# Kernel tuning notes

Measured on AMD Instinct MI355X. Metric: run time of the kernel, lower is better.

Reference implementation:

```python
import jax, jax.numpy as jnp
import numpy as np

N = 50000
E = 800000
HID = 128
OUT = 64
HEADS = 4
NEG_SLOPE = 0.2


def gat_layer(x, edge_index, W, att_src, att_dst, bias):
    """PyG-style GATConv: shared linear for src/dst, additive attention,
    self-loops, segment softmax over incoming edges, concat heads + bias."""
    n = x.shape[0]
    H, C = att_src.shape
    # add self loops (PyG default add_self_loops=True)
    loops = jnp.arange(n, dtype=edge_index.dtype)
    src = jnp.concatenate([edge_index[0], loops])  # message sources j
    dst = jnp.concatenate([edge_index[1], loops])  # aggregation targets i
    xl = (x @ W).reshape(n, H, C)                  # [N,H,C]
    a_s = jnp.einsum('nhc,hc->nh', xl, att_src)    # [N,H]
    a_d = jnp.einsum('nhc,hc->nh', xl, att_dst)    # [N,H]
    e = jax.nn.leaky_relu(a_s[src] + a_d[dst], NEG_SLOPE)   # [E',H]
    m = jax.ops.segment_max(e, dst, num_segments=n)         # stable softmax
    e = jnp.exp(e - m[dst])
    denom = jax.ops.segment_sum(e, dst, num_segments=n)
    alpha = e / (denom[dst] + 1e-16)                        # [E',H]
    msg = xl[src] * alpha[:, :, None]                       # [E',H,C]
    out = jax.ops.segment_sum(msg, dst, num_segments=n)     # [N,H,C]
    return out.reshape(n, H * C) + bias


def setup_inputs() -> dict:
    key = jax.random.key(0)
    ks = jax.random.split(key, 16)
    C = HID // HEADS  # per-head channels = 32
    x = jax.random.normal(ks[0], (N, HID), dtype=jnp.float32)
    edge_indices = jax.random.randint(ks[1], (3, 2, E), 0, N, dtype=jnp.int32)
    s = 0.1
    inp = {
        'x': x,
        'edge_indices': edge_indices,
        'W1': jax.random.normal(ks[2], (HID, HEADS * C), dtype=jnp.float32) * s,
        'as1': jax.random.normal(ks[3], (HEADS, C), dtype=jnp.float32) * s,
        'ad1': jax.random.normal(ks[4], (HEADS, C), dtype=jnp.float32) * s,
        'b1': jnp.zeros((HEADS * C,), dtype=jnp.float32),
        'W2': jax.random.normal(ks[5], (HID, HEADS * C), dtype=jnp.float32) * s,
        'as2': jax.random.normal(ks[6], (HEADS, C), dtype=jnp.float32) * s,
        'ad2': jax.random.normal(ks[7], (HEADS, C), dtype=jnp.float32) * s,
        'b2': jnp.zeros((HEADS * C,), dtype=jnp.float32),
        'W3': jax.random.normal(ks[8], (HID, OUT), dtype=jnp.float32) * s,
        'as3': jax.random.normal(ks[9], (1, OUT), dtype=jnp.float32) * s,
        'ad3': jax.random.normal(ks[10], (1, OUT), dtype=jnp.float32) * s,
        'b3': jnp.zeros((OUT,), dtype=jnp.float32),
    }
    return inp


def reference(x, edge_indices, W1, as1, ad1, b1, W2, as2, ad2, b2, W3, as3, ad3, b3):
    h = jax.nn.relu(gat_layer(x, edge_indices[0], W1, as1, ad1, b1))
    h = jax.nn.relu(gat_layer(h, edge_indices[1], W2, as2, ad2, b2))
    out = gat_layer(h, edge_indices[2], W3, as3, ad3, b3)  # no ReLU on last layer
    return out
```

## Files before the change

kernel.cpp:

```cpp
#include <hip/hip_runtime.h>

typedef unsigned short u16;
typedef unsigned int u32;

#define HID 128

static inline int cdiv(long long a, int b) { return (int)((a + b - 1) / b); }

__device__ __forceinline__ float bfbits(u32 u) { union { u32 u; float f; } c; c.u = u; return c.f; }
__device__ __forceinline__ u16 f2bf(float f) {
  union { float f; u32 u; } c; c.f = f;
  u32 u = c.u;
  return (u16)((u + 0x7fffu + ((u >> 16) & 1u)) >> 16);
}
__device__ __forceinline__ u32 pack2bf(float a, float b) {
  return (u32)f2bf(a) | ((u32)f2bf(b) << 16);
}

template <int COUT, int HEADS>
__global__ __launch_bounds__(256) void gemm_attn(
    const float* __restrict__ Hin, const float* __restrict__ W,
    const float* __restrict__ attS, const float* __restrict__ attD,
    u16* __restrict__ XL, float* __restrict__ aS, float* __restrict__ aD, int n) {
  constexpr int TN = COUT / 8;
  constexpr int TM = 256 / TN;
  constexpr int MT = TM * 8;
  constexpr int HALF = COUT / 2;
  constexpr int C = COUT / HEADS;
  constexpr bool SAMEHEAD = (HALF < C);

  __shared__ float xs[32][MT + 4];
  __shared__ float ws[32][COUT];

  int t = threadIdx.x;
  int tx = t % TN, ty = t / TN;
  int rowBase = blockIdx.x * MT;

  float acc[8][8];
#pragma unroll
  for (int r = 0; r < 8; ++r)
#pragma unroll
    for (int c = 0; c < 8; ++c) acc[r][c] = 0.f;

  for (int kb = 0; kb < 4; ++kb) {
    __syncthreads();
    {
      int kg = (t & 7) * 4;
#pragma unroll
      for (int pass = 0; pass < MT / 32; ++pass) {
        int rr = pass * 32 + (t >> 3);
        int grow = rowBase + rr;
        float4 v = make_float4(0.f, 0.f, 0.f, 0.f);
        if (grow < n) v = *(const float4*)(Hin + (size_t)grow * HID + kb * 32 + kg);
        xs[kg + 0][rr] = v.x;
        xs[kg + 1][rr] = v.y;
        xs[kg + 2][rr] = v.z;
        xs[kg + 3][rr] = v.w;
      }
    }
    {
      constexpr int WF = 32 * COUT / 256;
      const float* wp = W + (size_t)kb * 32 * COUT;
      float* wsf = &ws[0][0];
#pragma unroll
      for (int u = 0; u < WF; u += 4) {
        int idx = t * WF + u;
        *(float4*)(wsf + idx) = *(const float4*)(wp + idx);
      }
    }
    __syncthreads();
#pragma unroll 8
    for (int k = 0; k < 32; ++k) {
      const float4 xv0 = *(const float4*)&xs[k][ty * 8];
      const float4 xv1 = *(const float4*)&xs[k][ty * 8 + 4];
      const float4 wv0 = *(const float4*)&ws[k][tx * 4];
      const float4 wv1 = *(const float4*)&ws[k][HALF + tx * 4];
      const float xr[8] = {xv0.x, xv0.y, xv0.z, xv0.w, xv1.x, xv1.y, xv1.z, xv1.w};
      const float wc[8] = {wv0.x, wv0.y, wv0.z, wv0.w, wv1.x, wv1.y, wv1.z, wv1.w};
#pragma unroll
      for (int r = 0; r < 8; ++r)
#pragma unroll
        for (int c = 0; c < 8; ++c) acc[r][c] += xr[r] * wc[c];
    }
  }

  float sv[8], dv[8];
#pragma unroll
  for (int j = 0; j < 4; ++j) {
    sv[j] = attS[tx * 4 + j];
    sv[4 + j] = attS[HALF + tx * 4 + j];
    dv[j] = attD[tx * 4 + j];
    dv[4 + j] = attD[HALF + tx * 4 + j];
  }
  int row0 = rowBase + ty * 8;
  int hlo = (tx * 4) / C;
  int hhi = (HALF + tx * 4) / C;
  u32* XLo = (u32*)XL;
#pragma unroll
  for (int r = 0; r < 8; ++r) {
    int row = row0 + r;
    bool ok = (row < n);
    if (ok) {
      u32 lo01 = pack2bf(acc[r][0], acc[r][1]);
      u32 lo23 = pack2bf(acc[r][2], acc[r][3]);
      u32 hi01 = pack2bf(acc[r][4], acc[r][5]);
      u32 hi23 = pack2bf(acc[r][6], acc[r][7]);
      *(uint2*)(XLo + (size_t)row * (COUT / 2) + tx * 2) = make_uint2(lo01, lo23);
      *(uint2*)(XLo + (size_t)row * (COUT / 2) + COUT / 4 + tx * 2) = make_uint2(hi01, hi23);
    }
    float pslo = acc[r][0] * sv[0] + acc[r][1] * sv[1] + acc[r][2] * sv[2] + acc[r][3] * sv[3];
    float pshi = acc[r][4] * sv[4] + acc[r][5] * sv[5] + acc[r][6] * sv[6] + acc[r][7] * sv[7];
    float pdlo = acc[r][0] * dv[0] + acc[r][1] * dv[1] + acc[r][2] * dv[2] + acc[r][3] * dv[3];
    float pdhi = acc[r][4] * dv[4] + acc[r][5] * dv[5] + acc[r][6] * dv[6] + acc[r][7] * dv[7];
    if (SAMEHEAD) { pslo += pshi; pdlo += pdhi; }
#pragma unroll
    for (int mk = 1; mk < 8; mk <<= 1) {
      pslo += __shfl_xor(pslo, mk);
      pdlo += __shfl_xor(pdlo, mk);
      if (!SAMEHEAD) {
        pshi += __shfl_xor(pshi, mk);
        pdhi += __shfl_xor(pdhi, mk);
      }
    }
    if (((tx & 7) == 0) && ok) {
      aS[(size_t)row * HEADS + hlo] = pslo;
      aD[(size_t)row * HEADS + hlo] = pdlo;
      if (!SAMEHEAD) {
        aS[(size_t)row * HEADS + hhi] = pshi;
        aD[(size_t)row * HEADS + hhi] = pdhi;
      }
    }
  }
}

#define PSTR 16

__global__ __launch_bounds__(256) void bucket_hist(const int* __restrict__ ei,
                                                   int* __restrict__ cntP,
                                                   int e4, int rem, int E, int NB) {
  int L = blockIdx.y;
  const int* dst = ei + (size_t)(2 * L + 1) * E;
  __shared__ int cnt[256];
  int t = threadIdx.x;
  cnt[t] = 0;
  __syncthreads();
  int gbase = blockIdx.x * 1024 + t;
#pragma unroll
  for (int u = 0; u < 4; ++u) {
    int g = gbase + u * 256;
    if (g < e4) {
      int4 d = *(const int4*)(dst + g * 4);
      atomicAdd(&cnt[d.x >> 8], 1);
      atomicAdd(&cnt[d.y >> 8], 1);
      atomicAdd(&cnt[d.z >> 8], 1);
      atomicAdd(&cnt[d.w >> 8], 1);
    }
  }
  if (blockIdx.x == 0 && t < rem) atomicAdd(&cnt[dst[e4 * 4 + t] >> 8], 1);
  __syncthreads();
  int c = cnt[t];
  if (t < NB && c > 0) atomicAdd(&cntP[(L * NB + t) * PSTR], c);
}

__global__ __launch_bounds__(256) void bucket_scan(const int* __restrict__ cntP,
                                                   int* __restrict__ bucketOff,
                                                   int* __restrict__ curP, int NB, int E) {
  int L = blockIdx.x;
  int t = threadIdx.x;
  int lane = t & 63, wid = t >> 6;
  __shared__ int wpart[4];
  int v = (t < NB) ? cntP[(L * NB + t) * PSTR] : 0;
  int inc = v;
#pragma unroll
  for (int off = 1; off < 64; off <<= 1) {
    int w = __shfl_up(inc, (unsigned)off, 64);
    if (lane >= off) inc += w;
  }
  if (lane == 63) wpart[wid] = inc;
  __syncthreads();
  if (t == 0) {
    int a = 0;
#pragma unroll
    for (int k = 0; k < 4; ++k) { int tmp = wpart[k]; wpart[k] = a; a += tmp; }
  }
  __syncthreads();
  int ex = wpart[wid] + inc - v;
  if (t < NB) {
    bucketOff[L * (NB + 1) + t] = ex;
    curP[(L * NB + t) * PSTR] = ex;
  }
  if (t == 0) bucketOff[L * (NB + 1) + NB] = E;
}

__global__ __launch_bounds__(256) void bucket_scatter(const int* __restrict__ ei,
                                                      int* __restrict__ curP,
                                                      int2* __restrict__ pairsAll,
                                                      int e4, int rem, int E, int NB) {
  int L = blockIdx.y;
  const int* src = ei + (size_t)(2 * L) * E;
  const int* dst = src + E;
  int2* pairs = pairsAll + (size_t)L * E;
  __shared__ int cnt[256];
  __shared__ int baseS[256];
  int t = threadIdx.x;
  cnt[t] = 0;
  __syncthreads();

  int gbase = blockIdx.x * 1024 + t;
  int4 dv[4], sv[4];
  bool val[4];
#pragma unroll
  for (int u = 0; u < 4; ++u) {
    int g = gbase + u * 256;
    val[u] = (g < e4);
    if (val[u]) {
      dv[u] = *(const int4*)(dst + g * 4);
      sv[u] = *(const int4*)(src + g * 4);
      atomicAdd(&cnt[dv[u].x >> 8], 1);
      atomicAdd(&cnt[dv[u].y >> 8], 1);
      atomicAdd(&cnt[dv[u].z >> 8], 1);
      atomicAdd(&cnt[dv[u].w >> 8], 1);
    }
  }
  int tailS = 0, tailD = 0;
  bool hasTail = (blockIdx.x == 0 && t < rem);
  if (hasTail) {
    tailD = dst[e4 * 4 + t];
    tailS = src[e4 * 4 + t];
    atomicAdd(&cnt[tailD >> 8], 1);
  }
  __syncthreads();
  int c = cnt[t];
  if (t < NB && c > 0) baseS[t] = atomicAdd(&curP[(L * NB + t) * PSTR], c);
  __syncthreads();
  cnt[t] = 0;
  __syncthreads();
#pragma unroll
  for (int u = 0; u < 4; ++u) {
    if (val[u]) {
      int b, p;
      b = dv[u].x >> 8; p = atomicAdd(&cnt[b], 1); pairs[baseS[b] + p] = make_int2(sv[u].x, dv[u].x);
      b = dv[u].y >> 8; p = atomicAdd(&cnt[b], 1); pairs[baseS[b] + p] = make_int2(sv[u].y, dv[u].y);
      b = dv[u].z >> 8; p = atomicAdd(&cnt[b], 1); pairs[baseS[b] + p] = make_int2(sv[u].z, dv[u].z);
      b = dv[u].w >> 8; p = atomicAdd(&cnt[b], 1); pairs[baseS[b] + p] = make_int2(sv[u].w, dv[u].w);
    }
  }
  if (hasTail) {
    int b = tailD >> 8;
    int p = atomicAdd(&cnt[b], 1);
    pairs[baseS[b] + p] = make_int2(tailS, tailD);
  }
}

__global__ __launch_bounds__(256) void csr_finalize(const int2* __restrict__ pairsAll,
                                                    const int* __restrict__ bucketOff,
                                                    int* __restrict__ indptrAll,
                                                    int* __restrict__ srcIdxAll,
                                                    int N, int E, int NB) {
  int L = blockIdx.y, b = blockIdx.x;
  const int2* pairs = pairsAll + (size_t)L * E;
  int* indptr = indptrAll + (size_t)L * (N + 1);
  int* srcL = srcIdxAll + (size_t)L * (E + N);
  int base = b << 8;
  int nodes = min(256, N - base);
  int p0 = bucketOff[L * (NB + 1) + b];
  int p1 = bucketOff[L * (NB + 1) + b + 1];

  __shared__ int cnt[256];
  __shared__ int wpart[4];
  int t = threadIdx.x;
  int lane = t & 63, wid = t >> 6;
  cnt[t] = 0;
  __syncthreads();

  for (int i = p0 + t; i < p1; i += 256) atomicAdd(&cnt[pairs[i].y - base], 1);
  __syncthreads();

  int v = (t < nodes) ? cnt[t] + 1 : 0;
  int inc = v;
#pragma unroll
  for (int off = 1; off < 64; off <<= 1) {
    int w = __shfl_up(inc, (unsigned)off, 64);
    if (lane >= off) inc += w;
  }
  if (lane == 63) wpart[wid] = inc;
  __syncthreads();
  if (t == 0) {
    int a = 0;
#pragma unroll
    for (int k = 0; k < 4; ++k) { int tmp = wpart[k]; wpart[k] = a; a += tmp; }
  }
  __syncthreads();
  int ex = wpart[wid] + inc - v;
  __syncthreads();
  if (t < nodes) {
    int segStart = p0 + base + ex;
    indptr[base + t] = segStart;
    srcL[segStart] = base + t;
    cnt[t] = segStart + 1;
  }
  if (b == NB - 1 && t == 0) indptr[N] = E + N;
  __syncthreads();

  for (int i = p0 + t; i < p1; i += 256) {
    int2 pr = pairs[i];
    int p = atomicAdd(&cnt[pr.y - base], 1);
    srcL[p] = pr.x;
  }
}

template <int COUT, int HEADS, bool RELU>
__global__ __launch_bounds__(256) void aggregate(
    const u16* __restrict__ XL, const float* __restrict__ aS, const float* __restrict__ aD,
    const int* __restrict__ indptr, const int* __restrict__ srcIdx,
    const float* __restrict__ bias, float* __restrict__ outF, int n) {
  constexpr int VPL = COUT / 64;
  constexpr int C = COUT / HEADS;
  int wave = (blockIdx.x * blockDim.x + threadIdx.x) >> 6;
  if (wave >= n) return;
  int lane = threadIdx.x & 63;
  int i = wave;
  int col = lane * VPL;
  int h = col / C;
  float ad = aD[i * HEADS + h];
  float s = 0.f, acc0 = 0.f, acc1 = 0.f;
  int e0 = indptr[i], e1 = indptr[i + 1];
  int idx = e0;
  const u32* XL32 = (const u32*)XL;

  for (; idx + 8 <= e1; idx += 8) {
    int j[8];
#pragma unroll
    for (int u = 0; u < 8; ++u) j[u] = srcIdx[idx + u];
    float a[8];
#pragma unroll
    for (int u = 0; u < 8; ++u) a[u] = aS[j[u] * HEADS + h];
    if (VPL == 2) {
      u32 px[8];
#pragma unroll
      for (int u = 0; u < 8; ++u) px[u] = XL32[j[u] * (COUT / 2) + lane];
#pragma unroll
      for (int u = 0; u < 8; ++u) {
        float l = a[u] + ad;
        l = (l >= 0.f) ? l : 0.2f * l;
        float el = __expf(fminf(l, 60.f));
        s += el;
        acc0 += el * bfbits(px[u] << 16);
        acc1 += el * bfbits(px[u] & 0xffff0000u);
      }
    } else {
      u16 px[8];
#pragma unroll
      for (int u = 0; u < 8; ++u) px[u] = XL[j[u] * COUT + lane];
#pragma unroll
      for (int u = 0; u < 8; ++u) {
        float l = a[u] + ad;
        l = (l >= 0.f) ? l : 0.2f * l;
        float el = __expf(fminf(l, 60.f));
        s += el;
        acc0 += el * bfbits(((u32)px[u]) << 16);
      }
    }
  }
  for (; idx < e1; ++idx) {
    int j = srcIdx[idx];
    float l = aS[j * HEADS + h] + ad;
    l = (l >= 0.f) ? l : 0.2f * l;
    float el = __expf(fminf(l, 60.f));
    s += el;
    if (VPL == 2) {
      u32 px = XL32[j * (COUT / 2) + lane];
      acc0 += el * bfbits(px << 16);
      acc1 += el * bfbits(px & 0xffff0000u);
    } else {
      acc0 += el * bfbits(((u32)XL[j * COUT + lane]) << 16);
    }
  }

  float inv = 1.f / (s + 1e-16f);
  float o0 = acc0 * inv + bias[col];
  if (RELU) o0 = fmaxf(o0, 0.f);
  if (VPL == 2) {
    float o1 = acc1 * inv + bias[col + 1];
    if (RELU) o1 = fmaxf(o1, 0.f);
    *(float2*)(outF + ((size_t)i * COUT + col)) = make_float2(o0, o1);
  } else {
    outF[(size_t)i * COUT + col] = o0;
  }
}

extern "C" void kernel_launch(void* const* d_in, const int* in_sizes, int n_in,
                              void* d_out, int out_size, void* d_ws, size_t ws_size,
                              hipStream_t stream) {
  const float* x = (const float*)d_in[0];
  const int* ei = (const int*)d_in[1];
  const float* W1 = (const float*)d_in[2];
  const float* as1 = (const float*)d_in[3];
  const float* ad1 = (const float*)d_in[4];
  const float* b1 = (const float*)d_in[5];
  const float* W2 = (const float*)d_in[6];
  const float* as2 = (const float*)d_in[7];
  const float* ad2 = (const float*)d_in[8];
  const float* b2 = (const float*)d_in[9];
  const float* W3 = (const float*)d_in[10];
  const float* as3 = (const float*)d_in[11];
  const float* ad3 = (const float*)d_in[12];
  const float* b3 = (const float*)d_in[13];

  int N = in_sizes[0] / HID;
  int E = in_sizes[1] / 6;
  int NB = cdiv(N, 256);

  char* w = (char*)d_ws;
  auto alloc = [&](size_t bytes) {
    void* q = (void*)w;
    w += (bytes + 255) & ~(size_t)255;
    return q;
  };
  float* bufH = (float*)alloc((size_t)N * HID * 4);
  u16* bufXL = (u16*)alloc((size_t)N * HID * 2);
  float* aS = (float*)alloc((size_t)N * 4 * 4);
  float* aD = (float*)alloc((size_t)N * 4 * 4);
  int* cntP = (int*)alloc((size_t)3 * NB * PSTR * 4);
  int* curP = (int*)alloc((size_t)3 * NB * PSTR * 4);
  int* bucketOff = (int*)alloc((size_t)3 * (NB + 1) * 4);
  int2* pairsAll = (int2*)alloc((size_t)3 * E * 8);
  int* indptrAll = (int*)alloc((size_t)3 * (N + 1) * 4);
  int* srcIdxAll = (int*)alloc((size_t)3 * (E + N) * 4);

  int e4 = E >> 2, rem = E & 3;
  int gx = cdiv(e4, 1024);

  hipMemsetAsync(cntP, 0, (size_t)3 * NB * PSTR * 4, stream);
  {
    dim3 g(gx, 3);
    bucket_hist<<<g, 256, 0, stream>>>(ei, cntP, e4, rem, E, NB);
  }
  bucket_scan<<<3, 256, 0, stream>>>(cntP, bucketOff, curP, NB, E);
  {
    dim3 g(gx, 3);
    bucket_scatter<<<g, 256, 0, stream>>>(ei, curP, pairsAll, e4, rem, E, NB);
  }
  {
    dim3 g(NB, 3);
    csr_finalize<<<g, 256, 0, stream>>>(pairsAll, bucketOff, indptrAll, srcIdxAll, N, E, NB);
  }

  gemm_attn<128, 4><<<cdiv(N, 128), 256, 0, stream>>>(x, W1, as1, ad1, bufXL, aS, aD, N);
  aggregate<128, 4, true><<<cdiv(N, 4), 256, 0, stream>>>(
      bufXL, aS, aD, indptrAll, srcIdxAll, b1, bufH, N);
  gemm_attn<128, 4><<<cdiv(N, 128), 256, 0, stream>>>(bufH, W2, as2, ad2, bufXL, aS, aD, N);
  aggregate<128, 4, true><<<cdiv(N, 4), 256, 0, stream>>>(
      bufXL, aS, aD, indptrAll + (N + 1), srcIdxAll + (size_t)(E + N), b2, bufH, N);
  gemm_attn<64, 1><<<cdiv(N, 256), 256, 0, stream>>>(bufH, W3, as3, ad3, bufXL, aS, aD, N);
  aggregate<64, 1, false><<<cdiv(N, 4), 256, 0, stream>>>(
      bufXL, aS, aD, indptrAll + 2 * (N + 1), srcIdxAll + (size_t)2 * (E + N), b3,
      (float*)d_out, N);
}
```

Before: 386.2 us.

## Split wave into edge groups with 16-byte loads and shuffle reduction in aggregate

The aggregation kernel now divides each 64-lane wave into several groups. Each group processes a different incoming edge, and each lane loads 8 bf16 features with one 128-bit load instead of 1–2 elements per lane across all 64 lanes. Partial sums and feature accumulators are combined with xor-shuffles across groups, and group 0 writes the output with float4 stores. This is meant to raise memory-level parallelism and cut per-edge instruction overhead on gathers. The cost is redundant exp work per group, a shuffle reduction at the end, and less explicit unrolling across edges.

```diff
diff --git a/kernel.cpp b/kernel.cpp
--- a/kernel.cpp
+++ b/kernel.cpp
@@ -314,78 +314,71 @@
     const u16* __restrict__ XL, const float* __restrict__ aS, const float* __restrict__ aD,
     const int* __restrict__ indptr, const int* __restrict__ srcIdx,
     const float* __restrict__ bias, float* __restrict__ outF, int n) {
-  constexpr int VPL = COUT / 64;
+  constexpr int VPL = 8;
+  constexpr int LPG = COUT / VPL;
+  constexpr int G = 64 / LPG;
   constexpr int C = COUT / HEADS;
   int wave = (blockIdx.x * blockDim.x + threadIdx.x) >> 6;
   if (wave >= n) return;
   int lane = threadIdx.x & 63;
+  int g = lane / LPG;
+  int cl = lane % LPG;
+  int col0 = cl * VPL;
+  int h = col0 / C;
   int i = wave;
-  int col = lane * VPL;
-  int h = col / C;
   float ad = aD[i * HEADS + h];
-  float s = 0.f, acc0 = 0.f, acc1 = 0.f;
+  float s = 0.f;
+  float acc[VPL];
+#pragma unroll
+  for (int v = 0; v < VPL; ++v) acc[v] = 0.f;
   int e0 = indptr[i], e1 = indptr[i + 1];
+  const u32* XL32 = (const u32*)XL;
+
+  auto doEdge = [&](int loadIdx, bool act) {
+    int j = srcIdx[loadIdx];
+    float a = aS[j * HEADS + h];
+    uint4 px = *(const uint4*)(XL32 + j * (COUT / 2) + cl * 4);
+    float l = a + ad;
+    l = (l >= 0.f) ? l : 0.2f * l;
+    float el = act ? __expf(fminf(l, 60.f)) : 0.f;
+    s += el;
+    acc[0] += el * bfbits(px.x << 16);
+    acc[1] += el * bfbits(px.x & 0xffff0000u);
+    acc[2] += el * bfbits(px.y << 16);
+    acc[3] += el * bfbits(px.y & 0xffff0000u);
+    acc[4] += el * bfbits(px.z << 16);
+    acc[5] += el * bfbits(px.z & 0xffff0000u);
+    acc[6] += el * bfbits(px.w << 16);
+    acc[7] += el * bfbits(px.w & 0xffff0000u);
+  };
+
   int idx = e0;
-  const u32* XL32 = (const u32*)XL;
-
-  for (; idx + 8 <= e1; idx += 8) {
-    int j[8];
-#pragma unroll
-    for (int u = 0; u < 8; ++u) j[u] = srcIdx[idx + u];
-    float a[8];
-#pragma unroll
-    for (int u = 0; u < 8; ++u) a[u] = aS[j[u] * HEADS + h];
-    if (VPL == 2) {
-      u32 px[8];
-#pragma unroll
-      for (int u = 0; u < 8; ++u) px[u] = XL32[j[u] * (COUT / 2) + lane];
-#pragma unroll
-      for (int u = 0; u < 8; ++u) {
-        float l = a[u] + ad;
-        l = (l >= 0.f) ? l : 0.2f * l;
-        float el = __expf(fminf(l, 60.f));
-        s += el;
-        acc0 += el * bfbits(px[u] << 16);
-        acc1 += el * bfbits(px[u] & 0xffff0000u);
-      }
-    } else {
-      u16 px[8];
-#pragma unroll
-      for (int u = 0; u < 8; ++u) px[u] = XL[j[u] * COUT + lane];
-#pragma unroll
-      for (int u = 0; u < 8; ++u) {
-        float l = a[u] + ad;
-        l = (l >= 0.f) ? l : 0.2f * l;
-        float el = __expf(fminf(l, 60.f));
-        s += el;
-        acc0 += el * bfbits(((u32)px[u]) << 16);
-      }
-    }
-  }
-  for (; idx < e1; ++idx) {
-    int j = srcIdx[idx];
-    float l = aS[j * HEADS + h] + ad;
-    l = (l >= 0.f) ? l : 0.2f * l;
-    float el = __expf(fminf(l, 60.f));
-    s += el;
-    if (VPL == 2) {
-      u32 px = XL32[j * (COUT / 2) + lane];
-      acc0 += el * bfbits(px << 16);
-      acc1 += el * bfbits(px & 0xffff0000u);
-    } else {
-      acc0 += el * bfbits(((u32)XL[j * COUT + lane]) << 16);
-    }
-  }
-
-  float inv = 1.f / (s + 1e-16f);
-  float o0 = acc0 * inv + bias[col];
-  if (RELU) o0 = fmaxf(o0, 0.f);
-  if (VPL == 2) {
-    float o1 = acc1 * inv + bias[col + 1];
-    if (RELU) o1 = fmaxf(o1, 0.f);
-    *(float2*)(outF + ((size_t)i * COUT + col)) = make_float2(o0, o1);
-  } else {
-    outF[(size_t)i * COUT + col] = o0;
+  for (; idx + 2 * G <= e1; idx += 2 * G) {
+    doEdge(idx + g, true);
+    doEdge(idx + G + g, true);
+  }
+  for (; idx + G <= e1; idx += G) doEdge(idx + g, true);
+  int r = e1 - idx;
+  if (r > 0) doEdge((g < r) ? (idx + g) : e0, g < r);
+
+#pragma unroll
+  for (int mk = LPG; mk < 64; mk <<= 1) {
+    s += __shfl_xor(s, mk);
+#pragma unroll
+    for (int v = 0; v < VPL; ++v) acc[v] += __shfl_xor(acc[v], mk);
+  }
+
+  if (g == 0) {
+    float inv = 1.f / (s + 1e-16f);
+    float o[VPL];
+#pragma unroll
+    for (int v = 0; v < VPL; ++v) {
+      o[v] = acc[v] * inv + bias[col0 + v];
+      if (RELU) o[v] = fmaxf(o[v], 0.f);
+    }
+    float* op = outF + (size_t)i * COUT + col0;
+    *(float4*)op = make_float4(o[0], o[1], o[2], o[3]);
+    *(float4*)(op + 4) = make_float4(o[4], o[5], o[6], o[7]);
   }
 }
 
```

New measurement: 357.1 us. -7.5%, faster.
